# Kernel optimization log

Measured on AMD Instinct MI355X. Metric: run time of the kernel, lower is better.

## Reference

```python
import jax, jax.numpy as jnp
import numpy as np

B, S, D, H, MAX_OBJ, N_IMGS = 256, 256, 256, 4, 50, 32


def setup_inputs() -> dict:
    key = jax.random.key(0)
    ks = jax.random.split(key, 8)
    std = 1.0 / np.sqrt(D)
    mk = lambda k: (jax.random.normal(k, (D, D), jnp.float32) * std)
    return {
        "batch_seq": jax.random.normal(ks[0], (B, S, D), jnp.float32),
        "img_ids": jax.random.randint(ks[1], (B,), 0, N_IMGS, jnp.int32),
        "Wq": mk(ks[2]), "Wk": mk(ks[3]), "Wv": mk(ks[4]), "Wo": mk(ks[5]),
        "bq": jnp.zeros((D,), jnp.float32), "bk": jnp.zeros((D,), jnp.float32),
        "bv": jnp.zeros((D,), jnp.float32), "bo": jnp.zeros((D,), jnp.float32),
        "obj_emb": jax.random.normal(ks[6], (MAX_OBJ, D), jnp.float32) * 0.02,
        "scale": jnp.ones((1,), jnp.float32) * 0.2,
    }


def reference(batch_seq, img_ids, Wq, Wk, Wv, Wo, bq, bk, bv, bo, obj_emb, scale):
    Bn, Sn, Dn = batch_seq.shape
    dh = Dn // H
    idx = jnp.arange(Bn)
    same = img_ids[:, None] == img_ids[None, :]          # (B, B) group membership
    rank = jnp.sum(same & (idx[None, :] < idx[:, None]), axis=1)  # position within group
    gsize = jnp.sum(same, axis=1)                         # group size per item

    # enhanced features: add rank-indexed object embedding (broadcast over seq)
    enh = batch_seq + scale * obj_emb[rank][:, None, :]   # (B, S, D)

    # MHA over the seq dimension, batched over B (eval mode, no dropout)
    q = (enh @ Wq + bq).reshape(Bn, Sn, H, dh)
    k = (enh @ Wk + bk).reshape(Bn, Sn, H, dh)
    v = (enh @ Wv + bv).reshape(Bn, Sn, H, dh)
    scores = jnp.einsum("bqhd,bkhd->bhqk", q, k) / float(np.sqrt(dh))
    attn = jax.nn.softmax(scores, axis=-1)
    ctx = jnp.einsum("bhqk,bkhd->bqhd", attn, v).reshape(Bn, Sn, Dn)
    att_out = ctx @ Wo + bo

    # residual; items in singleton groups are passed through unchanged
    return jnp.where((gsize > 1)[:, None, None], batch_seq + att_out, batch_seq)
```

## Files before the change

### kernel.cpp

```cpp
#include <hip/hip_runtime.h>

typedef __bf16 bf16x8 __attribute__((ext_vector_type(8)));
typedef float f32x4 __attribute__((ext_vector_type(4)));
typedef ushort u16x8 __attribute__((ext_vector_type(8)));

__device__ __forceinline__ float bf2f(ushort u) {
    union { unsigned int i; float f; } v; v.i = ((unsigned int)u) << 16; return v.f;
}
__device__ __forceinline__ ushort f2bf(float f) {
    union { float f; unsigned int i; } v; v.f = f;
    unsigned int i = v.i;
    return (ushort)((i + 0x7FFFu + ((i >> 16) & 1u)) >> 16);
}
__device__ __forceinline__ unsigned int addmul_bf2(unsigned int xs, unsigned int es, float sc) {
    float f0 = bf2f((ushort)(xs & 0xffffu)) + sc * bf2f((ushort)(es & 0xffffu));
    float f1 = bf2f((ushort)(xs >> 16))     + sc * bf2f((ushort)(es >> 16));
    return (unsigned int)f2bf(f0) | (((unsigned int)f2bf(f1)) << 16);
}

__global__ __launch_bounds__(256) void sniff_kernel(
    const unsigned int* __restrict__ bs_words, int* __restrict__ flag)
{
    const int t = threadIdx.x;
    int hit = 0;
    for (int i = 0; i < 64; ++i) {
        unsigned int w = bs_words[t * 64 + i];
        unsigned int e0 = (w >> 7)  & 0xffu;
        unsigned int e1 = (w >> 23) & 0xffu;
        if (e0 > 150u || e1 > 150u) hit = 1;
    }
    __shared__ int s;
    if (t == 0) s = 0;
    __syncthreads();
    if (hit) atomicOr(&s, 1);
    __syncthreads();
    if (t == 0) *flag = s;
}

__global__ __launch_bounds__(256) void prep_kernel(
    const int* __restrict__ flag,
    const void* __restrict__ Wq, const void* __restrict__ Wk,
    const void* __restrict__ Wv, const void* __restrict__ Wo,
    const void* __restrict__ c0, const void* __restrict__ c1,
    const void* __restrict__ c2, const void* __restrict__ c3,
    const void* __restrict__ c4, const void* __restrict__ scale_in,
    int* __restrict__ rank, int* __restrict__ gsize,
    ushort* __restrict__ Wqkv_t, ushort* __restrict__ Wo_t,
    float* __restrict__ bqkv_f, float* __restrict__ bo_f,
    float* __restrict__ scale_f)
{
    const int blk = blockIdx.x;
    const int t = threadIdx.x;
    const bool is_f32 = (*flag != 0);
    if (blk < 256) {
        const int k = blk;
        ushort q, kk, vv, oo;
        if (is_f32) {
            q  = f2bf(((const float*)Wq)[k * 256 + t]);
            kk = f2bf(((const float*)Wk)[k * 256 + t]);
            vv = f2bf(((const float*)Wv)[k * 256 + t]);
            oo = f2bf(((const float*)Wo)[k * 256 + t]);
        } else {
            q  = ((const ushort*)Wq)[k * 256 + t];
            kk = ((const ushort*)Wk)[k * 256 + t];
            vv = ((const ushort*)Wv)[k * 256 + t];
            oo = ((const ushort*)Wo)[k * 256 + t];
        }
        Wqkv_t[(size_t)t * 256 + k]         = q;
        Wqkv_t[(size_t)(256 + t) * 256 + k] = kk;
        Wqkv_t[(size_t)(512 + t) * 256 + k] = vv;
        Wo_t[(size_t)t * 256 + k]           = oo;
    } else {
        const void* cands[5] = {c0, c1, c2, c3, c4};
        __shared__ int cstat[5];
        if (t < 5) cstat[t] = 0;
        __syncthreads();
        #pragma unroll
        for (int c = 0; c < 5; ++c) {
            unsigned int wv = ((const unsigned int*)cands[c])[t];
            int fl = ((wv != 0u) ? 1 : 0) | ((wv >= 32u) ? 2 : 0);
            if (fl) atomicOr(&cstat[c], fl);
        }
        __syncthreads();
        int sel = 0;
        #pragma unroll
        for (int c = 4; c >= 0; --c)
            if (cstat[c] == 1) sel = c;
        const int* ids = (const int*)cands[sel];
        int bp[4];
        { int n = 0;
          #pragma unroll
          for (int c = 0; c < 5; ++c) if (c != sel) bp[n++] = c; }

        const int b = t;
        const int my = ids[b];
        int r = 0, g = 0;
        for (int j = 0; j < 256; ++j) {
            bool same = (ids[j] == my);
            r += (same && (j < b)) ? 1 : 0;
            g += same ? 1 : 0;
        }
        rank[b]  = (r > 49) ? 49 : r;
        gsize[b] = g;

        float vq, vk, vv2, vo2;
        if (is_f32) {
            vq  = ((const float*)cands[bp[0]])[t];
            vk  = ((const float*)cands[bp[1]])[t];
            vv2 = ((const float*)cands[bp[2]])[t];
            vo2 = ((const float*)cands[bp[3]])[t];
            if (t == 0) *scale_f = ((const float*)scale_in)[0];
        } else {
            vq  = bf2f(((const ushort*)cands[bp[0]])[t]);
            vk  = bf2f(((const ushort*)cands[bp[1]])[t]);
            vv2 = bf2f(((const ushort*)cands[bp[2]])[t]);
            vo2 = bf2f(((const ushort*)cands[bp[3]])[t]);
            if (t == 0) *scale_f = bf2f(((const ushort*)scale_in)[0]);
        }
        bqkv_f[t]       = vq;
        bqkv_f[256 + t] = vk;
        bqkv_f[512 + t] = vv2;
        bo_f[t]         = vo2;
    }
}

__global__ __launch_bounds__(256, 2) void qkv_half_kernel(
    const int* __restrict__ flag,
    const void* __restrict__ bs, const void* __restrict__ obj_emb,
    const float* __restrict__ scale_f, const ushort* __restrict__ Wqkv_t,
    const float* __restrict__ bqkv_f, const int* __restrict__ rank,
    int half,
    ushort* __restrict__ Qg, ushort* __restrict__ Kg, ushort* __restrict__ Vt)
{
    __shared__ __attribute__((aligned(16))) ushort A_lds[64 * 32];
    __shared__ __attribute__((aligned(16))) ushort B_lds[256 * 32];

    const int m0 = half * 32768 + blockIdx.y * 64;
    const int n0 = blockIdx.x * 256;
    const int b  = m0 >> 8;
    const int bl = b & 127;
    const int tid = threadIdx.x;
    const int w = tid >> 6, l = tid & 63, quad = l >> 4, l15 = l & 15;
    const bool is_f32 = (*flag != 0);
    const float sc = *scale_f;
    const int rk = rank[b];

    f32x4 acc[4][4];
    #pragma unroll
    for (int i = 0; i < 4; ++i)
        #pragma unroll
        for (int j = 0; j < 4; ++j) { f32x4 z = {0.f,0.f,0.f,0.f}; acc[i][j] = z; }

    const int arow = tid >> 2, ako = (tid & 3) * 8;

    for (int k0 = 0; k0 < 256; k0 += 32) {
        const size_t aoff = (((size_t)(m0 + arow)) << 8) + k0 + ako;
        if (is_f32) {
            const float* bsf = (const float*)bs;
            const float* ef  = (const float*)obj_emb + rk * 256 + k0 + ako;
            float4 x0 = *(const float4*)(bsf + aoff);
            float4 x1 = *(const float4*)(bsf + aoff + 4);
            float4 e0 = *(const float4*)(ef);
            float4 e1 = *(const float4*)(ef + 4);
            u16x8 o;
            o[0] = f2bf(x0.x + sc * e0.x); o[1] = f2bf(x0.y + sc * e0.y);
            o[2] = f2bf(x0.z + sc * e0.z); o[3] = f2bf(x0.w + sc * e0.w);
            o[4] = f2bf(x1.x + sc * e1.x); o[5] = f2bf(x1.y + sc * e1.y);
            o[6] = f2bf(x1.z + sc * e1.z); o[7] = f2bf(x1.w + sc * e1.w);
            *(u16x8*)&A_lds[arow * 32 + ako] = o;
        } else {
            const ushort* b16 = (const ushort*)bs;
            const ushort* ef  = (const ushort*)obj_emb + rk * 256 + k0 + ako;
            uint4 x = *(const uint4*)(b16 + aoff);
            uint4 e = *(const uint4*)ef;
            uint4 o;
            o.x = addmul_bf2(x.x, e.x, sc);
            o.y = addmul_bf2(x.y, e.y, sc);
            o.z = addmul_bf2(x.z, e.z, sc);
            o.w = addmul_bf2(x.w, e.w, sc);
            *(uint4*)&A_lds[arow * 32 + ako] = o;
        }
        #pragma unroll
        for (int i = 0; i < 4; ++i) {
            int f = tid + i * 256;
            int n = f >> 2, ko = (f & 3) * 8;
            *(uint4*)&B_lds[n * 32 + ko] =
                *(const uint4*)(Wqkv_t + (((size_t)(n0 + n)) << 8) + k0 + ko);
        }
        __syncthreads();
        bf16x8 a[4], bb[4];
        #pragma unroll
        for (int mt = 0; mt < 4; ++mt)
            a[mt] = *(const bf16x8*)&A_lds[(mt * 16 + l15) * 32 + quad * 8];
        #pragma unroll
        for (int nt = 0; nt < 4; ++nt)
            bb[nt] = *(const bf16x8*)&B_lds[(w * 64 + nt * 16 + l15) * 32 + quad * 8];
        #pragma unroll
        for (int mt = 0; mt < 4; ++mt)
            #pragma unroll
            for (int nt = 0; nt < 4; ++nt)
                acc[mt][nt] = __builtin_amdgcn_mfma_f32_16x16x32_bf16(
                    a[mt], bb[nt], acc[mt][nt], 0, 0, 0);
        __syncthreads();
    }

    #pragma unroll
    for (int nt = 0; nt < 4; ++nt) {
        const int n_g = n0 + w * 64 + nt * 16 + l15;
        const int seg = n_g >> 8;
        const int within = n_g & 255;
        const int h = within >> 6, d = within & 63;
        const float bias = bqkv_f[n_g];
        const size_t bh = (size_t)(bl * 4 + h);
        #pragma unroll
        for (int mt = 0; mt < 4; ++mt) {
            const int sbase = (m0 & 255) + mt * 16 + quad * 4;
            if (seg == 2) {
                ushort pk[4];
                #pragma unroll
                for (int r = 0; r < 4; ++r) pk[r] = f2bf(acc[mt][nt][r] + bias);
                *(ushort4*)(Vt + (bh * 64 + d) * 256 + sbase) =
                    make_ushort4(pk[0], pk[1], pk[2], pk[3]);
            } else if (seg == 0) {
                #pragma unroll
                for (int r = 0; r < 4; ++r)
                    Qg[(bh * 256 + sbase + r) * 64 + d] =
                        f2bf((acc[mt][nt][r] + bias) * 0.125f);
            } else {
                #pragma unroll
                for (int r = 0; r < 4; ++r)
                    Kg[(bh * 256 + sbase + r) * 64 + d] = f2bf(acc[mt][nt][r] + bias);
            }
        }
    }
}

__global__ __launch_bounds__(256, 2) void attn_half_kernel(
    const ushort* __restrict__ Qg, const ushort* __restrict__ Kg,
    const ushort* __restrict__ Vt, int half, ushort* __restrict__ ctx)
{
    __shared__ __attribute__((aligned(16))) ushort Pl[4][64 * 72];
    const int bh_l = blockIdx.x;
    const int b = half * 128 + (bh_l >> 2), h = bh_l & 3;
    const int tid = threadIdx.x;
    const int w = tid >> 6, l = tid & 63, quad = l >> 4, l15 = l & 15;

    const ushort* Qb = Qg + (size_t)bh_l * 256 * 64;
    const ushort* Kb = Kg + (size_t)bh_l * 256 * 64;
    const ushort* Vb = Vt + (size_t)bh_l * 64 * 256;

    bf16x8 qf[4][2];
    #pragma unroll
    for (int mt = 0; mt < 4; ++mt)
        #pragma unroll
        for (int ks = 0; ks < 2; ++ks) {
            int s = w * 64 + mt * 16 + l15;
            qf[mt][ks] = *(const bf16x8*)(Qb + (size_t)s * 64 + ks * 32 + quad * 8);
        }

    f32x4 O[4][4];
    float m_run[4][4], l_run[4][4];
    #pragma unroll
    for (int mt = 0; mt < 4; ++mt) {
        #pragma unroll
        for (int dt = 0; dt < 4; ++dt) { f32x4 z = {0.f,0.f,0.f,0.f}; O[mt][dt] = z; }
        #pragma unroll
        for (int r = 0; r < 4; ++r) { m_run[mt][r] = -1e30f; l_run[mt][r] = 0.f; }
    }

    for (int c = 0; c < 4; ++c) {
        f32x4 sacc[4][4];
        #pragma unroll
        for (int mt = 0; mt < 4; ++mt)
            #pragma unroll
            for (int nt = 0; nt < 4; ++nt) { f32x4 z = {0.f,0.f,0.f,0.f}; sacc[mt][nt] = z; }
        #pragma unroll
        for (int ks = 0; ks < 2; ++ks) {
            bf16x8 kf[4];
            #pragma unroll
            for (int nt = 0; nt < 4; ++nt) {
                int key = c * 64 + nt * 16 + l15;
                kf[nt] = *(const bf16x8*)(Kb + (size_t)key * 64 + ks * 32 + quad * 8);
            }
            #pragma unroll
            for (int mt = 0; mt < 4; ++mt)
                #pragma unroll
                for (int nt = 0; nt < 4; ++nt)
                    sacc[mt][nt] = __builtin_amdgcn_mfma_f32_16x16x32_bf16(
                        qf[mt][ks], kf[nt], sacc[mt][nt], 0, 0, 0);
        }

        #pragma unroll
        for (int mt = 0; mt < 4; ++mt) {
            f32x4 mx = sacc[mt][0];
            #pragma unroll
            for (int nt = 1; nt < 4; ++nt)
                #pragma unroll
                for (int r = 0; r < 4; ++r) mx[r] = fmaxf(mx[r], sacc[mt][nt][r]);
            #pragma unroll
            for (int r = 0; r < 4; ++r) {
                float v = mx[r];
                v = fmaxf(v, __shfl_xor(v, 1));
                v = fmaxf(v, __shfl_xor(v, 2));
                v = fmaxf(v, __shfl_xor(v, 4));
                v = fmaxf(v, __shfl_xor(v, 8));
                mx[r] = v;
            }
            float rs[4];
            #pragma unroll
            for (int r = 0; r < 4; ++r) {
                float nm = fmaxf(m_run[mt][r], mx[r]);
                float alpha = __expf(m_run[mt][r] - nm);
                m_run[mt][r] = nm;
                l_run[mt][r] *= alpha;
                float sum = 0.f;
                #pragma unroll
                for (int nt = 0; nt < 4; ++nt) {
                    float p = __expf(sacc[mt][nt][r] - nm);
                    sacc[mt][nt][r] = p;
                    sum += p;
                }
                rs[r] = sum;
                #pragma unroll
                for (int dt = 0; dt < 4; ++dt) O[mt][dt][r] *= alpha;
            }
            #pragma unroll
            for (int r = 0; r < 4; ++r) {
                float v = rs[r];
                v += __shfl_xor(v, 1);
                v += __shfl_xor(v, 2);
                v += __shfl_xor(v, 4);
                v += __shfl_xor(v, 8);
                l_run[mt][r] += v;
            }
            #pragma unroll
            for (int nt = 0; nt < 4; ++nt)
                #pragma unroll
                for (int r = 0; r < 4; ++r)
                    Pl[w][(mt * 16 + quad * 4 + r) * 72 + nt * 16 + l15] =
                        f2bf(sacc[mt][nt][r]);
        }

        #pragma unroll
        for (int ks = 0; ks < 2; ++ks) {
            bf16x8 pf[4], vf[4];
            #pragma unroll
            for (int mt = 0; mt < 4; ++mt)
                pf[mt] = *(const bf16x8*)&Pl[w][(mt * 16 + l15) * 72 + ks * 32 + quad * 8];
            #pragma unroll
            for (int dt = 0; dt < 4; ++dt)
                vf[dt] = *(const bf16x8*)(Vb + (size_t)(dt * 16 + l15) * 256 +
                                          c * 64 + ks * 32 + quad * 8);
            #pragma unroll
            for (int mt = 0; mt < 4; ++mt)
                #pragma unroll
                for (int dt = 0; dt < 4; ++dt)
                    O[mt][dt] = __builtin_amdgcn_mfma_f32_16x16x32_bf16(
                        pf[mt], vf[dt], O[mt][dt], 0, 0, 0);
        }
    }

    #pragma unroll
    for (int mt = 0; mt < 4; ++mt) {
        #pragma unroll
        for (int r = 0; r < 4; ++r) {
            float inv = 1.0f / l_run[mt][r];
            const int s = w * 64 + mt * 16 + quad * 4 + r;
            const size_t base = ((size_t)(b * 256 + s)) * 256 + h * 64;
            #pragma unroll
            for (int dt = 0; dt < 4; ++dt)
                ctx[base + dt * 16 + l15] = f2bf(O[mt][dt][r] * inv);
        }
    }
}

__global__ __launch_bounds__(256, 2) void out_kernel(
    const int* __restrict__ flag,
    const ushort* __restrict__ ctx, const ushort* __restrict__ Wo_t,
    const float* __restrict__ bo_f, const void* __restrict__ bs,
    const int* __restrict__ gsize, void* __restrict__ outv)
{
    __shared__ __attribute__((aligned(16))) ushort A_lds[64 * 32];
    __shared__ __attribute__((aligned(16))) ushort B_lds[256 * 32];

    const int m0 = blockIdx.x * 64;
    const int tid = threadIdx.x;
    const int w = tid >> 6, l = tid & 63, quad = l >> 4, l15 = l & 15;
    const int b = m0 >> 8;
    const bool pass = (gsize[b] <= 1);
    const bool is_f32 = (*flag != 0);

    f32x4 acc[4][4];
    #pragma unroll
    for (int i = 0; i < 4; ++i)
        #pragma unroll
        for (int j = 0; j < 4; ++j) { f32x4 z = {0.f,0.f,0.f,0.f}; acc[i][j] = z; }

    const int arow = tid >> 2, ako = (tid & 3) * 8;
    for (int k0 = 0; k0 < 256; k0 += 32) {
        *(uint4*)&A_lds[arow * 32 + ako] =
            *(const uint4*)(ctx + (((size_t)(m0 + arow)) << 8) + k0 + ako);
        #pragma unroll
        for (int i = 0; i < 4; ++i) {
            int f = tid + i * 256;
            int n = f >> 2, ko = (f & 3) * 8;
            *(uint4*)&B_lds[n * 32 + ko] =
                *(const uint4*)(Wo_t + (((size_t)n) << 8) + k0 + ko);
        }
        __syncthreads();
        bf16x8 a[4], bb[4];
        #pragma unroll
        for (int mt = 0; mt < 4; ++mt)
            a[mt] = *(const bf16x8*)&A_lds[(mt * 16 + l15) * 32 + quad * 8];
        #pragma unroll
        for (int nt = 0; nt < 4; ++nt)
            bb[nt] = *(const bf16x8*)&B_lds[(w * 64 + nt * 16 + l15) * 32 + quad * 8];
        #pragma unroll
        for (int mt = 0; mt < 4; ++mt)
            #pragma unroll
            for (int nt = 0; nt < 4; ++nt)
                acc[mt][nt] = __builtin_amdgcn_mfma_f32_16x16x32_bf16(
                    a[mt], bb[nt], acc[mt][nt], 0, 0, 0);
        __syncthreads();
    }

    #pragma unroll
    for (int nt = 0; nt < 4; ++nt) {
        const int n = w * 64 + nt * 16 + l15;
        const float bias = bo_f[n];
        #pragma unroll
        for (int mt = 0; mt < 4; ++mt)
            #pragma unroll
            for (int r = 0; r < 4; ++r) {
                int token = m0 + mt * 16 + quad * 4 + r;
                size_t idx = (((size_t)token) << 8) + n;
                float base = is_f32 ? ((const float*)bs)[idx]
                                    : bf2f(((const ushort*)bs)[idx]);
                float v = pass ? base : (base + acc[mt][nt][r] + bias);
                if (is_f32) ((float*)outv)[idx] = v;
                else        ((ushort*)outv)[idx] = f2bf(v);
            }
    }
}

extern "C" void kernel_launch(void* const* d_in, const int* in_sizes, int n_in,
                              void* d_out, int out_size, void* d_ws, size_t ws_size,
                              hipStream_t stream)
{
    int bs_i = -1, obj_i = -1, sc_i = -1;
    int w_i[4] = {2, 3, 4, 5}; int nw = 0;
    int c_i[5] = {1, 6, 7, 8, 9}; int nc = 0;
    for (int i = 0; i < n_in; ++i) {
        int s = in_sizes[i];
        if      (s == 16777216) bs_i = i;
        else if (s == 65536)  { if (nw < 4) w_i[nw] = i; ++nw; }
        else if (s == 12800)    obj_i = i;
        else if (s == 1)        sc_i = i;
        else if (s == 256)    { if (nc < 5) c_i[nc] = i; ++nc; }
    }
    if (bs_i < 0 || obj_i < 0 || sc_i < 0 || nw != 4 || nc != 5) {
        bs_i = 0; obj_i = 10; sc_i = 11;
        w_i[0] = 2; w_i[1] = 3; w_i[2] = 4; w_i[3] = 5;
        c_i[0] = 1; c_i[1] = 6; c_i[2] = 7; c_i[3] = 8; c_i[4] = 9;
    }
    const void* bs    = d_in[bs_i];
    const void* Wq    = d_in[w_i[0]];
    const void* Wk    = d_in[w_i[1]];
    const void* Wv    = d_in[w_i[2]];
    const void* Wo    = d_in[w_i[3]];
    const void* obj   = d_in[obj_i];
    const void* scale = d_in[sc_i];

    char* ws = (char*)d_ws;
    int*    flag    = (int*)ws;
    int*    rank    = (int*)(ws + 1024);
    int*    gsize   = (int*)(ws + 2048);
    float*  scale_f = (float*)(ws + 3072);
    float*  bqkv_f  = (float*)(ws + 4096);
    float*  bo_f    = (float*)(ws + 8192);
    ushort* Wqkv_t  = (ushort*)(ws + 16384);
    ushort* Wo_t    = (ushort*)(ws + 16384 + 393216);
    ushort* ctx     = (ushort*)(ws + (1 << 20));

    ushort* Qg = (ushort*)d_out;
    ushort* Kg = Qg + 8388608;
    ushort* Vt = Kg + 8388608;

    hipLaunchKernelGGL(sniff_kernel, dim3(1), dim3(256), 0, stream,
                       (const unsigned int*)bs, flag);
    hipLaunchKernelGGL(prep_kernel, dim3(257), dim3(256), 0, stream,
                       flag, Wq, Wk, Wv, Wo,
                       d_in[c_i[0]], d_in[c_i[1]], d_in[c_i[2]],
                       d_in[c_i[3]], d_in[c_i[4]], scale,
                       rank, gsize, Wqkv_t, Wo_t, bqkv_f, bo_f, scale_f);
    for (int half = 0; half < 2; ++half) {
        hipLaunchKernelGGL(qkv_half_kernel, dim3(3, 512), dim3(256), 0, stream,
                           flag, bs, obj, scale_f, Wqkv_t, bqkv_f, rank, half,
                           Qg, Kg, Vt);
        hipLaunchKernelGGL(attn_half_kernel, dim3(512), dim3(256), 0, stream,
                           Qg, Kg, Vt, half, ctx);
    }
    hipLaunchKernelGGL(out_kernel, dim3(1024), dim3(256), 0, stream,
                       flag, ctx, Wo_t, bo_f, bs, gsize, d_out);
}
```

Measured before the change: 334.6 us.

## Precompute enhanced input, use direct global-to-LDS loads, and unsplit QKV/attention passes

Moves the obj-embedding add and bf16 conversion into a separate elementwise kernel that writes an enhanced bf16 buffer. The QKV and output GEMMs then load tiles with global_load_lds (direct global-to-LDS copies) instead of going through registers. The two half-batch QKV/attention passes become single full-batch launches, with Q/K in the output buffer and V in a larger workspace. The attention kernel also hoists its V fragment loads ahead of the score computation. This costs an extra round trip of the enhanced tensor through memory and more workspace.

```diff
diff --git a/kernel.cpp b/kernel.cpp
--- a/kernel.cpp
+++ b/kernel.cpp
@@ -16,6 +16,11 @@
     float f0 = bf2f((ushort)(xs & 0xffffu)) + sc * bf2f((ushort)(es & 0xffffu));
     float f1 = bf2f((ushort)(xs >> 16))     + sc * bf2f((ushort)(es >> 16));
     return (unsigned int)f2bf(f0) | (((unsigned int)f2bf(f1)) << 16);
+}
+__device__ __forceinline__ void cp16(void* lds, const void* g) {
+    __builtin_amdgcn_global_load_lds(
+        (const __attribute__((address_space(1))) unsigned int*)g,
+        (__attribute__((address_space(3))) unsigned int*)lds, 16, 0, 0);
 }
 
 __global__ __launch_bounds__(256) void sniff_kernel(
@@ -124,26 +129,54 @@
     }
 }
 
-__global__ __launch_bounds__(256, 2) void qkv_half_kernel(
+__global__ __launch_bounds__(256) void enh_kernel(
     const int* __restrict__ flag,
     const void* __restrict__ bs, const void* __restrict__ obj_emb,
-    const float* __restrict__ scale_f, const ushort* __restrict__ Wqkv_t,
-    const float* __restrict__ bqkv_f, const int* __restrict__ rank,
-    int half,
+    const float* __restrict__ scale_f, const int* __restrict__ rank,
+    ushort* __restrict__ enh)
+{
+    const int idx = blockIdx.x * 256 + threadIdx.x;
+    const int e0 = idx * 8;
+    const int b = e0 >> 16;
+    const int col = e0 & 255;
+    const int rk = rank[b];
+    const float sc = *scale_f;
+    if (*flag != 0) {
+        const float* bsf = (const float*)bs + e0;
+        const float* ef  = (const float*)obj_emb + rk * 256 + col;
+        float4 x0 = *(const float4*)bsf, x1 = *(const float4*)(bsf + 4);
+        float4 ev0 = *(const float4*)ef, ev1 = *(const float4*)(ef + 4);
+        u16x8 o;
+        o[0] = f2bf(x0.x + sc * ev0.x); o[1] = f2bf(x0.y + sc * ev0.y);
+        o[2] = f2bf(x0.z + sc * ev0.z); o[3] = f2bf(x0.w + sc * ev0.w);
+        o[4] = f2bf(x1.x + sc * ev1.x); o[5] = f2bf(x1.y + sc * ev1.y);
+        o[6] = f2bf(x1.z + sc * ev1.z); o[7] = f2bf(x1.w + sc * ev1.w);
+        *(u16x8*)(enh + e0) = o;
+    } else {
+        uint4 x = *(const uint4*)((const ushort*)bs + e0);
+        uint4 e = *(const uint4*)((const ushort*)obj_emb + rk * 256 + col);
+        uint4 o;
+        o.x = addmul_bf2(x.x, e.x, sc);
+        o.y = addmul_bf2(x.y, e.y, sc);
+        o.z = addmul_bf2(x.z, e.z, sc);
+        o.w = addmul_bf2(x.w, e.w, sc);
+        *(uint4*)(enh + e0) = o;
+    }
+}
+
+__global__ __launch_bounds__(256, 2) void qkv_kernel(
+    const ushort* __restrict__ enh, const ushort* __restrict__ Wqkv_t,
+    const float* __restrict__ bqkv_f,
     ushort* __restrict__ Qg, ushort* __restrict__ Kg, ushort* __restrict__ Vt)
 {
     __shared__ __attribute__((aligned(16))) ushort A_lds[64 * 32];
     __shared__ __attribute__((aligned(16))) ushort B_lds[256 * 32];
 
-    const int m0 = half * 32768 + blockIdx.y * 64;
+    const int m0 = blockIdx.y * 64;
     const int n0 = blockIdx.x * 256;
     const int b  = m0 >> 8;
-    const int bl = b & 127;
     const int tid = threadIdx.x;
     const int w = tid >> 6, l = tid & 63, quad = l >> 4, l15 = l & 15;
-    const bool is_f32 = (*flag != 0);
-    const float sc = *scale_f;
-    const int rk = rank[b];
 
     f32x4 acc[4][4];
     #pragma unroll
@@ -151,41 +184,14 @@
         #pragma unroll
         for (int j = 0; j < 4; ++j) { f32x4 z = {0.f,0.f,0.f,0.f}; acc[i][j] = z; }
 
-    const int arow = tid >> 2, ako = (tid & 3) * 8;
-
     for (int k0 = 0; k0 < 256; k0 += 32) {
-        const size_t aoff = (((size_t)(m0 + arow)) << 8) + k0 + ako;
-        if (is_f32) {
-            const float* bsf = (const float*)bs;
-            const float* ef  = (const float*)obj_emb + rk * 256 + k0 + ako;
-            float4 x0 = *(const float4*)(bsf + aoff);
-            float4 x1 = *(const float4*)(bsf + aoff + 4);
-            float4 e0 = *(const float4*)(ef);
-            float4 e1 = *(const float4*)(ef + 4);
-            u16x8 o;
-            o[0] = f2bf(x0.x + sc * e0.x); o[1] = f2bf(x0.y + sc * e0.y);
-            o[2] = f2bf(x0.z + sc * e0.z); o[3] = f2bf(x0.w + sc * e0.w);
-            o[4] = f2bf(x1.x + sc * e1.x); o[5] = f2bf(x1.y + sc * e1.y);
-            o[6] = f2bf(x1.z + sc * e1.z); o[7] = f2bf(x1.w + sc * e1.w);
-            *(u16x8*)&A_lds[arow * 32 + ako] = o;
-        } else {
-            const ushort* b16 = (const ushort*)bs;
-            const ushort* ef  = (const ushort*)obj_emb + rk * 256 + k0 + ako;
-            uint4 x = *(const uint4*)(b16 + aoff);
-            uint4 e = *(const uint4*)ef;
-            uint4 o;
-            o.x = addmul_bf2(x.x, e.x, sc);
-            o.y = addmul_bf2(x.y, e.y, sc);
-            o.z = addmul_bf2(x.z, e.z, sc);
-            o.w = addmul_bf2(x.w, e.w, sc);
-            *(uint4*)&A_lds[arow * 32 + ako] = o;
-        }
+        cp16(&A_lds[tid * 8],
+             enh + ((size_t)(m0 + (tid >> 2)) << 8) + k0 + (tid & 3) * 8);
         #pragma unroll
         for (int i = 0; i < 4; ++i) {
-            int f = tid + i * 256;
-            int n = f >> 2, ko = (f & 3) * 8;
-            *(uint4*)&B_lds[n * 32 + ko] =
-                *(const uint4*)(Wqkv_t + (((size_t)(n0 + n)) << 8) + k0 + ko);
+            const int f = tid + i * 256;
+            cp16(&B_lds[f * 8],
+                 Wqkv_t + ((size_t)(n0 + (f >> 2)) << 8) + k0 + (f & 3) * 8);
         }
         __syncthreads();
         bf16x8 a[4], bb[4];
@@ -211,7 +217,7 @@
         const int within = n_g & 255;
         const int h = within >> 6, d = within & 63;
         const float bias = bqkv_f[n_g];
-        const size_t bh = (size_t)(bl * 4 + h);
+        const size_t bh = (size_t)(b * 4 + h);
         #pragma unroll
         for (int mt = 0; mt < 4; ++mt) {
             const int sbase = (m0 & 255) + mt * 16 + quad * 4;
@@ -235,19 +241,19 @@
     }
 }
 
-__global__ __launch_bounds__(256, 2) void attn_half_kernel(
+__global__ __launch_bounds__(256, 2) void attn_kernel(
     const ushort* __restrict__ Qg, const ushort* __restrict__ Kg,
-    const ushort* __restrict__ Vt, int half, ushort* __restrict__ ctx)
+    const ushort* __restrict__ Vt, ushort* __restrict__ ctx)
 {
     __shared__ __attribute__((aligned(16))) ushort Pl[4][64 * 72];
-    const int bh_l = blockIdx.x;
-    const int b = half * 128 + (bh_l >> 2), h = bh_l & 3;
+    const int bh = blockIdx.x;
+    const int b = bh >> 2, h = bh & 3;
     const int tid = threadIdx.x;
     const int w = tid >> 6, l = tid & 63, quad = l >> 4, l15 = l & 15;
 
-    const ushort* Qb = Qg + (size_t)bh_l * 256 * 64;
-    const ushort* Kb = Kg + (size_t)bh_l * 256 * 64;
-    const ushort* Vb = Vt + (size_t)bh_l * 64 * 256;
+    const ushort* Qb = Qg + (size_t)bh * 256 * 64;
+    const ushort* Kb = Kg + (size_t)bh * 256 * 64;
+    const ushort* Vb = Vt + (size_t)bh * 64 * 256;
 
     bf16x8 qf[4][2];
     #pragma unroll
@@ -269,6 +275,14 @@
     }
 
     for (int c = 0; c < 4; ++c) {
+        bf16x8 vf[2][4];
+        #pragma unroll
+        for (int ks = 0; ks < 2; ++ks)
+            #pragma unroll
+            for (int dt = 0; dt < 4; ++dt)
+                vf[ks][dt] = *(const bf16x8*)(Vb + (size_t)(dt * 16 + l15) * 256 +
+                                              c * 64 + ks * 32 + quad * 8);
+
         f32x4 sacc[4][4];
         #pragma unroll
         for (int mt = 0; mt < 4; ++mt)
@@ -343,20 +357,16 @@
 
         #pragma unroll
         for (int ks = 0; ks < 2; ++ks) {
-            bf16x8 pf[4], vf[4];
+            bf16x8 pf[4];
             #pragma unroll
             for (int mt = 0; mt < 4; ++mt)
                 pf[mt] = *(const bf16x8*)&Pl[w][(mt * 16 + l15) * 72 + ks * 32 + quad * 8];
             #pragma unroll
-            for (int dt = 0; dt < 4; ++dt)
-                vf[dt] = *(const bf16x8*)(Vb + (size_t)(dt * 16 + l15) * 256 +
-                                          c * 64 + ks * 32 + quad * 8);
-            #pragma unroll
             for (int mt = 0; mt < 4; ++mt)
                 #pragma unroll
                 for (int dt = 0; dt < 4; ++dt)
                     O[mt][dt] = __builtin_amdgcn_mfma_f32_16x16x32_bf16(
-                        pf[mt], vf[dt], O[mt][dt], 0, 0, 0);
+                        pf[mt], vf[ks][dt], O[mt][dt], 0, 0, 0);
         }
     }
 
@@ -396,16 +406,14 @@
         #pragma unroll
         for (int j = 0; j < 4; ++j) { f32x4 z = {0.f,0.f,0.f,0.f}; acc[i][j] = z; }
 
-    const int arow = tid >> 2, ako = (tid & 3) * 8;
     for (int k0 = 0; k0 < 256; k0 += 32) {
-        *(uint4*)&A_lds[arow * 32 + ako] =
-            *(const uint4*)(ctx + (((size_t)(m0 + arow)) << 8) + k0 + ako);
+        cp16(&A_lds[tid * 8],
+             ctx + ((size_t)(m0 + (tid >> 2)) << 8) + k0 + (tid & 3) * 8);
         #pragma unroll
         for (int i = 0; i < 4; ++i) {
-            int f = tid + i * 256;
-            int n = f >> 2, ko = (f & 3) * 8;
-            *(uint4*)&B_lds[n * 32 + ko] =
-                *(const uint4*)(Wo_t + (((size_t)n) << 8) + k0 + ko);
+            const int f = tid + i * 256;
+            cp16(&B_lds[f * 8],
+                 Wo_t + ((size_t)(f >> 2) << 8) + k0 + (f & 3) * 8);
         }
         __syncthreads();
         bf16x8 a[4], bb[4];
@@ -479,12 +487,13 @@
     float*  bqkv_f  = (float*)(ws + 4096);
     float*  bo_f    = (float*)(ws + 8192);
     ushort* Wqkv_t  = (ushort*)(ws + 16384);
-    ushort* Wo_t    = (ushort*)(ws + 16384 + 393216);
-    ushort* ctx     = (ushort*)(ws + (1 << 20));
+    ushort* Wo_t    = (ushort*)(ws + 409600);
+    ushort* enh     = (ushort*)(ws + ((size_t)1  << 20));
+    ushort* ctx     = (ushort*)(ws + ((size_t)33 << 20));
+    ushort* Vt      = (ushort*)(ws + ((size_t)65 << 20));
 
     ushort* Qg = (ushort*)d_out;
-    ushort* Kg = Qg + 8388608;
-    ushort* Vt = Kg + 8388608;
+    ushort* Kg = Qg + 16777216;
 
     hipLaunchKernelGGL(sniff_kernel, dim3(1), dim3(256), 0, stream,
                        (const unsigned int*)bs, flag);
@@ -493,13 +502,12 @@
                        d_in[c_i[0]], d_in[c_i[1]], d_in[c_i[2]],
                        d_in[c_i[3]], d_in[c_i[4]], scale,
                        rank, gsize, Wqkv_t, Wo_t, bqkv_f, bo_f, scale_f);
-    for (int half = 0; half < 2; ++half) {
-        hipLaunchKernelGGL(qkv_half_kernel, dim3(3, 512), dim3(256), 0, stream,
-                           flag, bs, obj, scale_f, Wqkv_t, bqkv_f, rank, half,
-                           Qg, Kg, Vt);
-        hipLaunchKernelGGL(attn_half_kernel, dim3(512), dim3(256), 0, stream,
-                           Qg, Kg, Vt, half, ctx);
-    }
+    hipLaunchKernelGGL(enh_kernel, dim3(8192), dim3(256), 0, stream,
+                       flag, bs, obj, scale_f, rank, enh);
+    hipLaunchKernelGGL(qkv_kernel, dim3(3, 1024), dim3(256), 0, stream,
+                       enh, Wqkv_t, bqkv_f, Qg, Kg, Vt);
+    hipLaunchKernelGGL(attn_kernel, dim3(1024), dim3(256), 0, stream,
+                       Qg, Kg, Vt, ctx);
     hipLaunchKernelGGL(out_kernel, dim3(1024), dim3(256), 0, stream,
                        flag, ctx, Wo_t, bo_f, bs, gsize, d_out);
 }
```

Measured after the change: 338.4 us. About the same (+1.1%).
